# Performance work log

Measured on AMD Instinct MI355X. Metric: run time of the kernel, lower is better.

Reference implementation:

```python
import jax, jax.numpy as jnp
import numpy as np

NUM_GRAPHS = 512


def setup_inputs() -> dict:
    key = jax.random.key(0)
    k1, k2, k3, k4, k5 = jax.random.split(key, 5)
    N, D = 131072, 512
    x = jax.random.normal(k1, (N, D), dtype=jnp.float32)
    graph_ptr = jnp.sort(jax.random.randint(k2, (N,), 0, NUM_GRAPHS, dtype=jnp.int64))
    # Linear(dim, dim) params (kaiming-ish scale) and query vector
    W = jax.random.normal(k3, (D, D), dtype=jnp.float32) / np.sqrt(D)
    b = jax.random.normal(k4, (D,), dtype=jnp.float32) * 0.01
    query = jax.random.normal(k5, (D,), dtype=jnp.float32)
    return {"x": x, "graph_ptr": graph_ptr, "W": W, "b": b, "query": query}


def reference(x, graph_ptr, W, b, query):
    # gate: Linear + Tanh, then score = g @ query  -> [N]
    g = jnp.tanh(x @ W.T + b)
    score = g @ query
    seg = graph_ptr.astype(jnp.int32)
    # segmented, numerically-stable softmax over nodes of each graph
    seg_max = jax.ops.segment_max(score, seg, num_segments=NUM_GRAPHS)  # [G]
    # empty segments give -inf max; they have no nodes so gather is safe
    e = jnp.exp(score - seg_max[seg])                                   # [N]
    denom = jax.ops.segment_sum(e, seg, num_segments=NUM_GRAPHS)        # [G]
    attn = e / jnp.where(denom[seg] == 0, 1.0, denom[seg])              # [N]
    # weighted scatter-sum of node features per graph -> [G, D]
    out = jax.ops.segment_sum(attn[:, None] * x, seg, num_segments=NUM_GRAPHS)
    return out
```

## Files before the change

### kernel.cpp

```cpp
#include <hip/hip_runtime.h>

typedef _Float16 f16x8 __attribute__((ext_vector_type(8)));
typedef short short8 __attribute__((ext_vector_type(8)));
typedef float f32x16 __attribute__((ext_vector_type(16)));

#define DD 512
#define NG 512

typedef __attribute__((address_space(3))) void lds_void;
typedef __attribute__((address_space(1))) void glb_void;

static __device__ __forceinline__ void gload_lds16(const void* g, void* l) {
  __builtin_amdgcn_global_load_lds((const glb_void*)g, (lds_void*)l, 16, 0, 0);
}

#define WAITV(n) asm volatile("s_waitcnt vmcnt(" #n ") lgkmcnt(0)" ::: "memory")
#define MEMFENCE asm volatile("" ::: "memory")

static __device__ __forceinline__ float fast_tanh(float v) {
  float e = __expf(2.0f * v);
  return 1.0f - 2.0f * __builtin_amdgcn_rcpf(e + 1.0f);
}

__global__ __launch_bounds__(256) void k_convert_w(const float* __restrict__ W,
                                                   unsigned char* __restrict__ Whl) {
  int t = blockIdx.x * 256 + threadIdx.x;
  int r512 = t >> 6, kg = t & 63;
  int ny = r512 >> 8, col = r512 & 255;
  int ct = col >> 5, c31 = col & 31;
  int kt = kg >> 1, khalf = kg & 1;
  const float* p = W + (size_t)r512 * DD + kg * 8;
  short8 h;
#pragma unroll
  for (int j = 0; j < 8; ++j) {
    _Float16 hh = (_Float16)p[j];
    h[j] = (short)__builtin_bit_cast(unsigned short, hh);
  }
  unsigned char* dst = Whl + (size_t)ny * 262144 + (size_t)kt * 8192 +
                       ct * 1024 + (khalf * 32 + c31) * 16;
  *(short8*)dst = h;
}

__global__ __launch_bounds__(256, 3) void k_gemm_score(
    const float* __restrict__ x, const unsigned char* __restrict__ Whl,
    const float* __restrict__ bias, const float* __restrict__ query,
    float* __restrict__ score_part, int N) {
  __shared__ unsigned char ldsB[3][8192];
  __shared__ unsigned char ldsA[3][8192];
  __shared__ float comb[2][128];
  const int tid = threadIdx.x;
  const int wave = tid >> 6;
  const int lane = tid & 63;
  const int l31 = lane & 31;
  const int kh = lane >> 5;
  const int rg = wave >> 1;
  const int cg = wave & 1;
  const int ny = blockIdx.x;
  const int brow0 = blockIdx.y * 128;

  const unsigned char* wsrc = Whl + (size_t)ny * 262144 +
                              (size_t)wave * 2048 + (size_t)lane * 16;

  const int c0 = wave * 128 + lane;
  const int c1 = c0 + 64;
  const int s0c = c0 ^ ((c0 >> 3) & 7);
  const int s1c = c1 ^ ((c1 >> 3) & 7);
  const float* asrc0 = x + (size_t)(brow0 + (s0c >> 2)) * DD + (s0c & 3) * 4;
  const float* asrc1 = x + (size_t)(brow0 + (s1c >> 2)) * DD + (s1c & 3) * 4;

  int aoff[2][2];
#pragma unroll
  for (int f = 0; f < 2; ++f) {
    const int row = rg * 64 + f * 32 + l31;
    const int u = row * 4 + 2 * kh;
    const int m = (u >> 3) & 7;
    aoff[f][0] = (u ^ m) * 16;
    aoff[f][1] = ((u + 1) ^ m) * 16;
  }

  f32x16 acc[2][4];
#pragma unroll
  for (int f = 0; f < 2; ++f)
#pragma unroll
    for (int j = 0; j < 4; ++j)
#pragma unroll
      for (int r = 0; r < 16; ++r) acc[f][j][r] = 0.f;

#pragma unroll
  for (int s = 0; s < 2; ++s) {
#pragma unroll
    for (int i = 0; i < 2; ++i)
      gload_lds16(wsrc + (size_t)s * 8192 + i * 1024, &ldsB[s][wave * 2048 + i * 1024]);
    gload_lds16(asrc0 + s * 16, &ldsA[s][wave * 2048]);
    gload_lds16(asrc1 + s * 16, &ldsA[s][wave * 2048 + 1024]);
    MEMFENCE;
  }

  for (int kt = 0; kt < 32; ++kt) {
    if (kt == 31) WAITV(0); else WAITV(4);
    __builtin_amdgcn_s_barrier();
    MEMFENCE;

    if (kt < 30) {
      const int s = (kt + 2) % 3;
      const unsigned char* src = wsrc + (size_t)(kt + 2) * 8192;
#pragma unroll
      for (int i = 0; i < 2; ++i)
        gload_lds16(src + i * 1024, &ldsB[s][wave * 2048 + i * 1024]);
      gload_lds16(asrc0 + (kt + 2) * 16, &ldsA[s][wave * 2048]);
      gload_lds16(asrc1 + (kt + 2) * 16, &ldsA[s][wave * 2048 + 1024]);
    }
    MEMFENCE;

    const int slot = kt % 3;
    const unsigned char* ab = &ldsA[slot][0];
    const unsigned char* bb = &ldsB[slot][lane * 16 + cg * 4096];

    f16x8 ah[2];
#pragma unroll
    for (int f = 0; f < 2; ++f) {
      const float4 a0 = *(const float4*)(ab + aoff[f][0]);
      const float4 a1 = *(const float4*)(ab + aoff[f][1]);
      float af[8] = {a0.x, a0.y, a0.z, a0.w, a1.x, a1.y, a1.z, a1.w};
#pragma unroll
      for (int j = 0; j < 8; ++j) ah[f][j] = (_Float16)af[j];
    }

    __builtin_amdgcn_s_setprio(1);
#pragma unroll
    for (int j = 0; j < 4; ++j) {
      f16x8 bh = *(const f16x8*)(bb + j * 1024);
#pragma unroll
      for (int f = 0; f < 2; ++f)
        acc[f][j] = __builtin_amdgcn_mfma_f32_32x32x16_f16(ah[f], bh, acc[f][j], 0, 0, 0);
    }
    __builtin_amdgcn_s_setprio(0);
  }

  float sp[2][16];
#pragma unroll
  for (int f = 0; f < 2; ++f)
#pragma unroll
    for (int r = 0; r < 16; ++r) sp[f][r] = 0.f;
#pragma unroll
  for (int j = 0; j < 4; ++j) {
    const int col = ny * 256 + (cg * 4 + j) * 32 + l31;
    const float bb2 = bias[col];
    const float qq = query[col];
#pragma unroll
    for (int f = 0; f < 2; ++f)
#pragma unroll
      for (int r = 0; r < 16; ++r)
        sp[f][r] += fast_tanh(acc[f][j][r] + bb2) * qq;
  }
#pragma unroll
  for (int f = 0; f < 2; ++f)
#pragma unroll
    for (int r = 0; r < 16; ++r) {
      float v = sp[f][r];
      v += __shfl_xor(v, 1);
      v += __shfl_xor(v, 2);
      v += __shfl_xor(v, 4);
      v += __shfl_xor(v, 8);
      v += __shfl_xor(v, 16);
      if (l31 == 0)
        comb[cg][rg * 64 + f * 32 + (r & 3) + 8 * (r >> 2) + 4 * kh] = v;
    }
  __syncthreads();
  if (tid < 128)
    score_part[(size_t)ny * N + brow0 + tid] = comb[0][tid] + comb[1][tid];
}

__global__ __launch_bounds__(256) void k_softmax_out(
    const float* __restrict__ x, const void* __restrict__ segp,
    const float* __restrict__ sp0, const float* __restrict__ sp1,
    float* __restrict__ out, int N) {
  const int g = blockIdx.x;
  const int tid = threadIdx.x;

  const long long probe = ((const long long*)segp)[N / 2 - 1];
  const bool is64 = ((unsigned long long)probe < (unsigned long long)NG);
  const long long* s64 = (const long long*)segp;
  const int* s32 = (const int*)segp;

  int s0, s1;
  {
    int lo = 0, hi = N;
    while (lo < hi) {
      int m = (lo + hi) >> 1;
      long long v = is64 ? s64[m] : (long long)s32[m];
      if (v < (long long)g) lo = m + 1; else hi = m;
    }
    s0 = lo;
    lo = s0; hi = N;
    while (lo < hi) {
      int m = (lo + hi) >> 1;
      long long v = is64 ? s64[m] : (long long)s32[m];
      if (v < (long long)(g + 1)) lo = m + 1; else hi = m;
    }
    s1 = lo;
  }

  __shared__ float red[4];
  __shared__ float wbuf[512];

  float lm = -INFINITY;
  for (int i = s0 + tid; i < s1; i += 256) lm = fmaxf(lm, sp0[i] + sp1[i]);
#pragma unroll
  for (int m = 1; m < 64; m <<= 1) lm = fmaxf(lm, __shfl_xor(lm, m));
  if ((tid & 63) == 0) red[tid >> 6] = lm;
  __syncthreads();
  const float mx = fmaxf(fmaxf(red[0], red[1]), fmaxf(red[2], red[3]));
  __syncthreads();

  float ls = 0.f;
  for (int i = s0 + tid; i < s1; i += 256) ls += expf(sp0[i] + sp1[i] - mx);
#pragma unroll
  for (int m = 1; m < 64; m <<= 1) ls += __shfl_xor(ls, m);
  if ((tid & 63) == 0) red[tid >> 6] = ls;
  __syncthreads();
  const float sum = red[0] + red[1] + red[2] + red[3];
  const float inv = sum > 0.f ? 1.0f / sum : 0.f;

  float a0 = 0.f, a1 = 0.f;
  const int c = tid * 2;
  for (int base = s0; base < s1; base += 512) {
    const int cnt = min(512, s1 - base);
    __syncthreads();
    for (int i = tid; i < cnt; i += 256)
      wbuf[i] = expf(sp0[base + i] + sp1[base + i] - mx) * inv;
    __syncthreads();
#pragma unroll 4
    for (int j = 0; j < cnt; ++j) {
      const float w = wbuf[j];
      const float2 xv = *(const float2*)(x + (size_t)(base + j) * DD + c);
      a0 = fmaf(w, xv.x, a0);
      a1 = fmaf(w, xv.y, a1);
    }
  }
  float* op = out + (size_t)g * DD + c;
  op[0] = a0;
  op[1] = a1;
}

extern "C" void kernel_launch(void* const* d_in, const int* in_sizes, int n_in,
                              void* d_out, int out_size, void* d_ws, size_t ws_size,
                              hipStream_t stream) {
  const float* x = (const float*)d_in[0];
  const void* seg = d_in[1];
  const float* W = (const float*)d_in[2];
  const float* b = (const float*)d_in[3];
  const float* q = (const float*)d_in[4];
  float* out = (float*)d_out;
  const int N = in_sizes[0] / DD;

  unsigned char* Whl = (unsigned char*)d_ws;
  float* sp0 = (float*)(Whl + 524288);
  float* sp1 = sp0 + N;

  k_convert_w<<<128, 256, 0, stream>>>(W, Whl);
  dim3 grid(2, N / 128);
  k_gemm_score<<<grid, 256, 0, stream>>>(x, Whl, b, q, sp0, N);
  k_softmax_out<<<NG, 256, 0, stream>>>(x, seg, sp0, sp1, out, N);
}
```

Baseline: 183.9 us.

## Halve GEMM row tile to 64 and use packed f16 conversion

The score GEMM kernel now handles 64 rows per block instead of 128. This halves the A-tile LDS buffers and the accumulators, and raises the occupancy hint from 3 to 4 blocks. The fp32-to-fp16 conversion of A now uses packed cvt_pkrtz, which rounds toward zero instead of to nearest. The smaller tile is meant to raise occupancy and wave count, at the cost of halving B-tile reuse per block and so doubling W traffic from L2.

```diff
diff --git a/kernel.cpp b/kernel.cpp
--- a/kernel.cpp
+++ b/kernel.cpp
@@ -1,6 +1,8 @@
 #include <hip/hip_runtime.h>
 
 typedef _Float16 f16x8 __attribute__((ext_vector_type(8)));
+typedef __fp16 fp16v2 __attribute__((ext_vector_type(2)));
+typedef _Float16 f16v2 __attribute__((ext_vector_type(2)));
 typedef short short8 __attribute__((ext_vector_type(8)));
 typedef float f32x16 __attribute__((ext_vector_type(16)));
 
@@ -16,6 +18,11 @@
 
 #define WAITV(n) asm volatile("s_waitcnt vmcnt(" #n ") lgkmcnt(0)" ::: "memory")
 #define MEMFENCE asm volatile("" ::: "memory")
+
+static __device__ __forceinline__ f16v2 pk16(float a, float b) {
+  fp16v2 p = __builtin_amdgcn_cvt_pkrtz(a, b);
+  return __builtin_bit_cast(f16v2, p);
+}
 
 static __device__ __forceinline__ float fast_tanh(float v) {
   float e = __expf(2.0f * v);
@@ -41,13 +48,13 @@
   *(short8*)dst = h;
 }
 
-__global__ __launch_bounds__(256, 3) void k_gemm_score(
+__global__ __launch_bounds__(256, 4) void k_gemm_score(
     const float* __restrict__ x, const unsigned char* __restrict__ Whl,
     const float* __restrict__ bias, const float* __restrict__ query,
     float* __restrict__ score_part, int N) {
   __shared__ unsigned char ldsB[3][8192];
-  __shared__ unsigned char ldsA[3][8192];
-  __shared__ float comb[2][128];
+  __shared__ unsigned char ldsA[3][4096];
+  __shared__ float comb[2][64];
   const int tid = threadIdx.x;
   const int wave = tid >> 6;
   const int lane = tid & 63;
@@ -56,48 +63,41 @@
   const int rg = wave >> 1;
   const int cg = wave & 1;
   const int ny = blockIdx.x;
-  const int brow0 = blockIdx.y * 128;
+  const int brow0 = blockIdx.y * 64;
 
   const unsigned char* wsrc = Whl + (size_t)ny * 262144 +
                               (size_t)wave * 2048 + (size_t)lane * 16;
 
-  const int c0 = wave * 128 + lane;
-  const int c1 = c0 + 64;
+  const int c0 = wave * 64 + lane;
   const int s0c = c0 ^ ((c0 >> 3) & 7);
-  const int s1c = c1 ^ ((c1 >> 3) & 7);
   const float* asrc0 = x + (size_t)(brow0 + (s0c >> 2)) * DD + (s0c & 3) * 4;
-  const float* asrc1 = x + (size_t)(brow0 + (s1c >> 2)) * DD + (s1c & 3) * 4;
-
-  int aoff[2][2];
-#pragma unroll
-  for (int f = 0; f < 2; ++f) {
-    const int row = rg * 64 + f * 32 + l31;
+
+  int aoff0, aoff1;
+  {
+    const int row = rg * 32 + l31;
     const int u = row * 4 + 2 * kh;
     const int m = (u >> 3) & 7;
-    aoff[f][0] = (u ^ m) * 16;
-    aoff[f][1] = ((u + 1) ^ m) * 16;
-  }
-
-  f32x16 acc[2][4];
-#pragma unroll
-  for (int f = 0; f < 2; ++f)
-#pragma unroll
-    for (int j = 0; j < 4; ++j)
-#pragma unroll
-      for (int r = 0; r < 16; ++r) acc[f][j][r] = 0.f;
+    aoff0 = (u ^ m) * 16;
+    aoff1 = ((u + 1) ^ m) * 16;
+  }
+
+  f32x16 acc[4];
+#pragma unroll
+  for (int j = 0; j < 4; ++j)
+#pragma unroll
+    for (int r = 0; r < 16; ++r) acc[j][r] = 0.f;
 
 #pragma unroll
   for (int s = 0; s < 2; ++s) {
 #pragma unroll
     for (int i = 0; i < 2; ++i)
       gload_lds16(wsrc + (size_t)s * 8192 + i * 1024, &ldsB[s][wave * 2048 + i * 1024]);
-    gload_lds16(asrc0 + s * 16, &ldsA[s][wave * 2048]);
-    gload_lds16(asrc1 + s * 16, &ldsA[s][wave * 2048 + 1024]);
+    gload_lds16(asrc0 + s * 16, &ldsA[s][wave * 1024]);
     MEMFENCE;
   }
 
   for (int kt = 0; kt < 32; ++kt) {
-    if (kt == 31) WAITV(0); else WAITV(4);
+    if (kt == 31) WAITV(0); else WAITV(3);
     __builtin_amdgcn_s_barrier();
     MEMFENCE;
 
@@ -107,8 +107,7 @@
 #pragma unroll
       for (int i = 0; i < 2; ++i)
         gload_lds16(src + i * 1024, &ldsB[s][wave * 2048 + i * 1024]);
-      gload_lds16(asrc0 + (kt + 2) * 16, &ldsA[s][wave * 2048]);
-      gload_lds16(asrc1 + (kt + 2) * 16, &ldsA[s][wave * 2048 + 1024]);
+      gload_lds16(asrc0 + (kt + 2) * 16, &ldsA[s][wave * 1024]);
     }
     MEMFENCE;
 
@@ -116,58 +115,52 @@
     const unsigned char* ab = &ldsA[slot][0];
     const unsigned char* bb = &ldsB[slot][lane * 16 + cg * 4096];
 
-    f16x8 ah[2];
-#pragma unroll
-    for (int f = 0; f < 2; ++f) {
-      const float4 a0 = *(const float4*)(ab + aoff[f][0]);
-      const float4 a1 = *(const float4*)(ab + aoff[f][1]);
-      float af[8] = {a0.x, a0.y, a0.z, a0.w, a1.x, a1.y, a1.z, a1.w};
-#pragma unroll
-      for (int j = 0; j < 8; ++j) ah[f][j] = (_Float16)af[j];
+    const float4 a0 = *(const float4*)(ab + aoff0);
+    const float4 a1 = *(const float4*)(ab + aoff1);
+    f16x8 ah;
+    {
+      f16v2 p;
+      p = pk16(a0.x, a0.y); ah[0] = p[0]; ah[1] = p[1];
+      p = pk16(a0.z, a0.w); ah[2] = p[0]; ah[3] = p[1];
+      p = pk16(a1.x, a1.y); ah[4] = p[0]; ah[5] = p[1];
+      p = pk16(a1.z, a1.w); ah[6] = p[0]; ah[7] = p[1];
     }
 
     __builtin_amdgcn_s_setprio(1);
 #pragma unroll
     for (int j = 0; j < 4; ++j) {
       f16x8 bh = *(const f16x8*)(bb + j * 1024);
-#pragma unroll
-      for (int f = 0; f < 2; ++f)
-        acc[f][j] = __builtin_amdgcn_mfma_f32_32x32x16_f16(ah[f], bh, acc[f][j], 0, 0, 0);
+      acc[j] = __builtin_amdgcn_mfma_f32_32x32x16_f16(ah, bh, acc[j], 0, 0, 0);
     }
     __builtin_amdgcn_s_setprio(0);
   }
 
-  float sp[2][16];
-#pragma unroll
-  for (int f = 0; f < 2; ++f)
-#pragma unroll
-    for (int r = 0; r < 16; ++r) sp[f][r] = 0.f;
+  float sp[16];
+#pragma unroll
+  for (int r = 0; r < 16; ++r) sp[r] = 0.f;
 #pragma unroll
   for (int j = 0; j < 4; ++j) {
     const int col = ny * 256 + (cg * 4 + j) * 32 + l31;
     const float bb2 = bias[col];
     const float qq = query[col];
 #pragma unroll
-    for (int f = 0; f < 2; ++f)
-#pragma unroll
-      for (int r = 0; r < 16; ++r)
-        sp[f][r] += fast_tanh(acc[f][j][r] + bb2) * qq;
-  }
-#pragma unroll
-  for (int f = 0; f < 2; ++f)
-#pragma unroll
-    for (int r = 0; r < 16; ++r) {
-      float v = sp[f][r];
-      v += __shfl_xor(v, 1);
-      v += __shfl_xor(v, 2);
-      v += __shfl_xor(v, 4);
-      v += __shfl_xor(v, 8);
-      v += __shfl_xor(v, 16);
-      if (l31 == 0)
-        comb[cg][rg * 64 + f * 32 + (r & 3) + 8 * (r >> 2) + 4 * kh] = v;
-    }
-  __syncthreads();
-  if (tid < 128)
+    for (int r = 0; r < 16; ++r)
+      sp[r] += fast_tanh(acc[j][r] + bb2) * qq;
+  }
+  __syncthreads();
+#pragma unroll
+  for (int r = 0; r < 16; ++r) {
+    float v = sp[r];
+    v += __shfl_xor(v, 1);
+    v += __shfl_xor(v, 2);
+    v += __shfl_xor(v, 4);
+    v += __shfl_xor(v, 8);
+    v += __shfl_xor(v, 16);
+    if (l31 == 0)
+      comb[cg][rg * 32 + (r & 3) + 8 * (r >> 2) + 4 * kh] = v;
+  }
+  __syncthreads();
+  if (tid < 64)
     score_part[(size_t)ny * N + brow0 + tid] = comb[0][tid] + comb[1][tid];
 }
 
@@ -259,7 +252,7 @@
   float* sp1 = sp0 + N;
 
   k_convert_w<<<128, 256, 0, stream>>>(W, Whl);
-  dim3 grid(2, N / 128);
+  dim3 grid(2, N / 64);
   k_gemm_score<<<grid, 256, 0, stream>>>(x, Whl, b, q, sp0, N);
   k_softmax_out<<<NG, 256, 0, stream>>>(x, seg, sp0, sp1, out, N);
 }
```

New measurement: 182.0 us. About the same (-1.0%).

## Load x tiles directly into registers instead of staging through LDS

Applied to the files above, without the earlier changes.

The GEMM kernel now reads the fp32 x operand straight from global memory into registers, double-buffered across two k-steps, and converts it with packed round-toward-zero fp16 conversions. Only W still goes through the three-stage LDS ring. This drops the LDS staging of x and its swizzled reads, removes lgkmcnt from the wait, and lowers the occupancy hint from 3 to 2. The cost is higher register pressure and less coalesced per-lane global loads of 32-byte chunks. Issuing loads for k-steps past the end wraps them to valid addresses, so some redundant traffic is issued.

```diff
diff --git a/kernel.cpp b/kernel.cpp
--- a/kernel.cpp
+++ b/kernel.cpp
@@ -1,6 +1,8 @@
 #include <hip/hip_runtime.h>
 
 typedef _Float16 f16x8 __attribute__((ext_vector_type(8)));
+typedef __fp16 fp16v2 __attribute__((ext_vector_type(2)));
+typedef _Float16 f16v2 __attribute__((ext_vector_type(2)));
 typedef short short8 __attribute__((ext_vector_type(8)));
 typedef float f32x16 __attribute__((ext_vector_type(16)));
 
@@ -14,8 +16,13 @@
   __builtin_amdgcn_global_load_lds((const glb_void*)g, (lds_void*)l, 16, 0, 0);
 }
 
-#define WAITV(n) asm volatile("s_waitcnt vmcnt(" #n ") lgkmcnt(0)" ::: "memory")
+#define WAITV(n) asm volatile("s_waitcnt vmcnt(" #n ")" ::: "memory")
 #define MEMFENCE asm volatile("" ::: "memory")
+
+static __device__ __forceinline__ f16v2 pk16(float a, float b) {
+  fp16v2 p = __builtin_amdgcn_cvt_pkrtz(a, b);
+  return __builtin_bit_cast(f16v2, p);
+}
 
 static __device__ __forceinline__ float fast_tanh(float v) {
   float e = __expf(2.0f * v);
@@ -41,12 +48,11 @@
   *(short8*)dst = h;
 }
 
-__global__ __launch_bounds__(256, 3) void k_gemm_score(
+__global__ __launch_bounds__(256, 2) void k_gemm_score(
     const float* __restrict__ x, const unsigned char* __restrict__ Whl,
     const float* __restrict__ bias, const float* __restrict__ query,
     float* __restrict__ score_part, int N) {
   __shared__ unsigned char ldsB[3][8192];
-  __shared__ unsigned char ldsA[3][8192];
   __shared__ float comb[2][128];
   const int tid = threadIdx.x;
   const int wave = tid >> 6;
@@ -60,23 +66,8 @@
 
   const unsigned char* wsrc = Whl + (size_t)ny * 262144 +
                               (size_t)wave * 2048 + (size_t)lane * 16;
-
-  const int c0 = wave * 128 + lane;
-  const int c1 = c0 + 64;
-  const int s0c = c0 ^ ((c0 >> 3) & 7);
-  const int s1c = c1 ^ ((c1 >> 3) & 7);
-  const float* asrc0 = x + (size_t)(brow0 + (s0c >> 2)) * DD + (s0c & 3) * 4;
-  const float* asrc1 = x + (size_t)(brow0 + (s1c >> 2)) * DD + (s1c & 3) * 4;
-
-  int aoff[2][2];
-#pragma unroll
-  for (int f = 0; f < 2; ++f) {
-    const int row = rg * 64 + f * 32 + l31;
-    const int u = row * 4 + 2 * kh;
-    const int m = (u >> 3) & 7;
-    aoff[f][0] = (u ^ m) * 16;
-    aoff[f][1] = ((u + 1) ^ m) * 16;
-  }
+  const float* xp0 = x + (size_t)(brow0 + rg * 64 + l31) * DD + kh * 8;
+  const float* xp1 = xp0 + (size_t)32 * DD;
 
   f32x16 acc[2][4];
 #pragma unroll
@@ -86,55 +77,65 @@
 #pragma unroll
       for (int r = 0; r < 16; ++r) acc[f][j][r] = 0.f;
 
-#pragma unroll
-  for (int s = 0; s < 2; ++s) {
-#pragma unroll
-    for (int i = 0; i < 2; ++i)
-      gload_lds16(wsrc + (size_t)s * 8192 + i * 1024, &ldsB[s][wave * 2048 + i * 1024]);
-    gload_lds16(asrc0 + s * 16, &ldsA[s][wave * 2048]);
-    gload_lds16(asrc1 + s * 16, &ldsA[s][wave * 2048 + 1024]);
-    MEMFENCE;
-  }
-
-  for (int kt = 0; kt < 32; ++kt) {
-    if (kt == 31) WAITV(0); else WAITV(4);
-    __builtin_amdgcn_s_barrier();
-    MEMFENCE;
-
-    if (kt < 30) {
-      const int s = (kt + 2) % 3;
-      const unsigned char* src = wsrc + (size_t)(kt + 2) * 8192;
-#pragma unroll
-      for (int i = 0; i < 2; ++i)
-        gload_lds16(src + i * 1024, &ldsB[s][wave * 2048 + i * 1024]);
-      gload_lds16(asrc0 + (kt + 2) * 16, &ldsA[s][wave * 2048]);
-      gload_lds16(asrc1 + (kt + 2) * 16, &ldsA[s][wave * 2048 + 1024]);
-    }
-    MEMFENCE;
-
-    const int slot = kt % 3;
-    const unsigned char* ab = &ldsA[slot][0];
-    const unsigned char* bb = &ldsB[slot][lane * 16 + cg * 4096];
-
-    f16x8 ah[2];
-#pragma unroll
-    for (int f = 0; f < 2; ++f) {
-      const float4 a0 = *(const float4*)(ab + aoff[f][0]);
-      const float4 a1 = *(const float4*)(ab + aoff[f][1]);
-      float af[8] = {a0.x, a0.y, a0.z, a0.w, a1.x, a1.y, a1.z, a1.w};
-#pragma unroll
-      for (int j = 0; j < 8; ++j) ah[f][j] = (_Float16)af[j];
-    }
-
-    __builtin_amdgcn_s_setprio(1);
-#pragma unroll
-    for (int j = 0; j < 4; ++j) {
-      f16x8 bh = *(const f16x8*)(bb + j * 1024);
-#pragma unroll
-      for (int f = 0; f < 2; ++f)
-        acc[f][j] = __builtin_amdgcn_mfma_f32_32x32x16_f16(ah[f], bh, acc[f][j], 0, 0, 0);
-    }
-    __builtin_amdgcn_s_setprio(0);
+#define ISSUE_A(BUF, KT)                                   \
+  do {                                                     \
+    const int km_ = (KT) & 31;                             \
+    BUF[0] = *(const float4*)(xp0 + km_ * 16);             \
+    BUF[1] = *(const float4*)(xp0 + km_ * 16 + 4);         \
+    BUF[2] = *(const float4*)(xp1 + km_ * 16);             \
+    BUF[3] = *(const float4*)(xp1 + km_ * 16 + 4);         \
+  } while (0)
+
+#define ISSUE_B(KT)                                                       \
+  do {                                                                    \
+    const int sl_ = (KT) % 3;                                             \
+    const unsigned char* sb_ = wsrc + (size_t)((KT) & 31) * 8192;         \
+    gload_lds16(sb_, &ldsB[sl_][wave * 2048]);                            \
+    gload_lds16(sb_ + 1024, &ldsB[sl_][wave * 2048 + 1024]);              \
+  } while (0)
+
+  float4 aP[4], aQ[4];
+  ISSUE_A(aP, 0); ISSUE_B(0); MEMFENCE;
+  ISSUE_A(aQ, 1); ISSUE_B(1); MEMFENCE;
+
+#define BODY(KT, CUR)                                                     \
+  do {                                                                    \
+    WAITV(6);                                     \
+    __builtin_amdgcn_s_barrier();                                         \
+    MEMFENCE;                                                             \
+              \
+    f16x8 ah0, ah1;                                                       \
+    {                                                                     \
+      f16v2 p_;                                                           \
+      p_ = pk16(CUR[0].x, CUR[0].y); ah0[0] = p_[0]; ah0[1] = p_[1];      \
+      p_ = pk16(CUR[0].z, CUR[0].w); ah0[2] = p_[0]; ah0[3] = p_[1];      \
+      p_ = pk16(CUR[1].x, CUR[1].y); ah0[4] = p_[0]; ah0[5] = p_[1];      \
+      p_ = pk16(CUR[1].z, CUR[1].w); ah0[6] = p_[0]; ah0[7] = p_[1];      \
+      p_ = pk16(CUR[2].x, CUR[2].y); ah1[0] = p_[0]; ah1[1] = p_[1];      \
+      p_ = pk16(CUR[2].z, CUR[2].w); ah1[2] = p_[0]; ah1[3] = p_[1];      \
+      p_ = pk16(CUR[3].x, CUR[3].y); ah1[4] = p_[0]; ah1[5] = p_[1];      \
+      p_ = pk16(CUR[3].z, CUR[3].w); ah1[6] = p_[0]; ah1[7] = p_[1];      \
+    }                                                                     \
+    MEMFENCE;                                                             \
+    ISSUE_A(CUR, (KT) + 2);                                               \
+    ISSUE_B((KT) + 2);                                                    \
+    MEMFENCE;                                                             \
+    const unsigned char* bb_ = &ldsB[(KT) % 3][lane * 16 + cg * 4096];    \
+    __builtin_amdgcn_s_setprio(1);                                        \
+    _Pragma("unroll")                                                     \
+    for (int j = 0; j < 4; ++j) {                                         \
+      f16x8 bh_ = *(const f16x8*)(bb_ + j * 1024);                        \
+      acc[0][j] = __builtin_amdgcn_mfma_f32_32x32x16_f16(ah0, bh_, acc[0][j], 0, 0, 0); \
+      acc[1][j] = __builtin_amdgcn_mfma_f32_32x32x16_f16(ah1, bh_, acc[1][j], 0, 0, 0); \
+    }                                                                     \
+    __builtin_amdgcn_s_setprio(0);                                        \
+  } while (0)
+
+#pragma unroll 1
+  for (int it = 0; it < 16; ++it) {
+    const int kt0 = it * 2;
+    BODY(kt0, aP);
+    BODY(kt0 + 1, aQ);
   }
 
   float sp[2][16];
@@ -153,6 +154,7 @@
       for (int r = 0; r < 16; ++r)
         sp[f][r] += fast_tanh(acc[f][j][r] + bb2) * qq;
   }
+  __syncthreads();
 #pragma unroll
   for (int f = 0; f < 2; ++f)
 #pragma unroll
```

After: 233.0 us. 1.27x slower.

## Keep a 128-column fp16 W slice resident in LDS and stream x through registers

Applied to the files above, without the earlier changes.

Each block now loads a full 128-column fp16 slice of W (128 KB) into LDS once, instead of streaming W tiles through a triple-buffered pipeline. The x rows are prefetched into registers two K-steps ahead, packed to fp16 with cvt_pkrtz, and written to a small per-wave LDS buffer. Blocks grow to 512 threads and the output columns are split four ways, so the softmax kernel now sums four partial scores. The aim is to cut W reload traffic and barrier overhead inside the K loop. The cost is that x is read four times instead of twice, and the large LDS footprint limits occupancy.

```diff
diff --git a/kernel.cpp b/kernel.cpp
--- a/kernel.cpp
+++ b/kernel.cpp
@@ -1,6 +1,9 @@
 #include <hip/hip_runtime.h>
 
 typedef _Float16 f16x8 __attribute__((ext_vector_type(8)));
+typedef _Float16 f16x4 __attribute__((ext_vector_type(4)));
+typedef __fp16 fp16v2 __attribute__((ext_vector_type(2)));
+typedef _Float16 f16v2 __attribute__((ext_vector_type(2)));
 typedef short short8 __attribute__((ext_vector_type(8)));
 typedef float f32x16 __attribute__((ext_vector_type(16)));
 
@@ -14,8 +17,10 @@
   __builtin_amdgcn_global_load_lds((const glb_void*)g, (lds_void*)l, 16, 0, 0);
 }
 
-#define WAITV(n) asm volatile("s_waitcnt vmcnt(" #n ") lgkmcnt(0)" ::: "memory")
-#define MEMFENCE asm volatile("" ::: "memory")
+static __device__ __forceinline__ f16v2 pk16(float a, float b) {
+  fp16v2 p = __builtin_amdgcn_cvt_pkrtz(a, b);
+  return __builtin_bit_cast(f16v2, p);
+}
 
 static __device__ __forceinline__ float fast_tanh(float v) {
   float e = __expf(2.0f * v);
@@ -26,8 +31,8 @@
                                                    unsigned char* __restrict__ Whl) {
   int t = blockIdx.x * 256 + threadIdx.x;
   int r512 = t >> 6, kg = t & 63;
-  int ny = r512 >> 8, col = r512 & 255;
-  int ct = col >> 5, c31 = col & 31;
+  int cq = r512 >> 7, rq = r512 & 127;
+  int ct = rq >> 5, c31 = rq & 31;
   int kt = kg >> 1, khalf = kg & 1;
   const float* p = W + (size_t)r512 * DD + kg * 8;
   short8 h;
@@ -36,47 +41,37 @@
     _Float16 hh = (_Float16)p[j];
     h[j] = (short)__builtin_bit_cast(unsigned short, hh);
   }
-  unsigned char* dst = Whl + (size_t)ny * 262144 + (size_t)kt * 8192 +
+  unsigned char* dst = Whl + (size_t)cq * 131072 + (size_t)kt * 4096 +
                        ct * 1024 + (khalf * 32 + c31) * 16;
   *(short8*)dst = h;
 }
 
-__global__ __launch_bounds__(256, 3) void k_gemm_score(
+__global__ __launch_bounds__(512, 2) void k_gemm_score(
     const float* __restrict__ x, const unsigned char* __restrict__ Whl,
     const float* __restrict__ bias, const float* __restrict__ query,
     float* __restrict__ score_part, int N) {
-  __shared__ unsigned char ldsB[3][8192];
-  __shared__ unsigned char ldsA[3][8192];
-  __shared__ float comb[2][128];
+  __shared__ unsigned char ldsW[131072];
+  __shared__ unsigned char ldsA[8][2048];
   const int tid = threadIdx.x;
   const int wave = tid >> 6;
   const int lane = tid & 63;
   const int l31 = lane & 31;
   const int kh = lane >> 5;
-  const int rg = wave >> 1;
-  const int cg = wave & 1;
-  const int ny = blockIdx.x;
-  const int brow0 = blockIdx.y * 128;
-
-  const unsigned char* wsrc = Whl + (size_t)ny * 262144 +
-                              (size_t)wave * 2048 + (size_t)lane * 16;
-
-  const int c0 = wave * 128 + lane;
-  const int c1 = c0 + 64;
-  const int s0c = c0 ^ ((c0 >> 3) & 7);
-  const int s1c = c1 ^ ((c1 >> 3) & 7);
-  const float* asrc0 = x + (size_t)(brow0 + (s0c >> 2)) * DD + (s0c & 3) * 4;
-  const float* asrc1 = x + (size_t)(brow0 + (s1c >> 2)) * DD + (s1c & 3) * 4;
-
-  int aoff[2][2];
-#pragma unroll
-  for (int f = 0; f < 2; ++f) {
-    const int row = rg * 64 + f * 32 + l31;
-    const int u = row * 4 + 2 * kh;
-    const int m = (u >> 3) & 7;
-    aoff[f][0] = (u ^ m) * 16;
-    aoff[f][1] = ((u + 1) ^ m) * 16;
-  }
+  const int cq = blockIdx.x;
+  const int brow0 = blockIdx.y * 512;
+
+  {
+    const unsigned char* wsrc = Whl + (size_t)cq * 131072 + (size_t)tid * 16;
+#pragma unroll
+    for (int i = 0; i < 16; ++i)
+      gload_lds16(wsrc + i * 8192, &ldsW[tid * 16 + i * 8192]);
+  }
+
+  const float* asrc = x + (size_t)(brow0 + wave * 64 + (lane >> 2)) * DD + (lane & 3) * 4;
+  unsigned char* awr = &ldsA[wave][(lane >> 2) * 32 + (lane & 3) * 8];
+  const unsigned char* ard0 = &ldsA[wave][l31 * 32 + kh * 16];
+  const unsigned char* ard1 = &ldsA[wave][(32 + l31) * 32 + kh * 16];
+  const unsigned char* wb = &ldsW[lane * 16];
 
   f32x16 acc[2][4];
 #pragma unroll
@@ -86,55 +81,46 @@
 #pragma unroll
       for (int r = 0; r < 16; ++r) acc[f][j][r] = 0.f;
 
-#pragma unroll
-  for (int s = 0; s < 2; ++s) {
-#pragma unroll
-    for (int i = 0; i < 2; ++i)
-      gload_lds16(wsrc + (size_t)s * 8192 + i * 1024, &ldsB[s][wave * 2048 + i * 1024]);
-    gload_lds16(asrc0 + s * 16, &ldsA[s][wave * 2048]);
-    gload_lds16(asrc1 + s * 16, &ldsA[s][wave * 2048 + 1024]);
-    MEMFENCE;
-  }
-
+  float4 aR[2][4];
+#pragma unroll
+  for (int j = 0; j < 4; ++j) aR[0][j] = *(const float4*)(asrc + j * 16 * DD);
+#pragma unroll
+  for (int j = 0; j < 4; ++j) aR[1][j] = *(const float4*)(asrc + j * 16 * DD + 16);
+
+#define AWRITE(S)                                                      \
+  do {                                                                 \
+    _Pragma("unroll")                                                  \
+    for (int j = 0; j < 4; ++j) {                                      \
+      f16v2 p0_ = pk16(aR[S][j].x, aR[S][j].y);                        \
+      f16v2 p1_ = pk16(aR[S][j].z, aR[S][j].w);                        \
+      f16x4 v_ = {p0_[0], p0_[1], p1_[0], p1_[1]};                     \
+      *(f16x4*)(awr + j * 512) = v_;                                   \
+    }                                                                  \
+  } while (0)
+
+  asm volatile("s_waitcnt vmcnt(0)" ::: "memory");
+  AWRITE(0);
+#pragma unroll
+  for (int j = 0; j < 4; ++j) aR[0][j] = *(const float4*)(asrc + j * 16 * DD + 32);
+  __syncthreads();
+
+#pragma unroll 2
   for (int kt = 0; kt < 32; ++kt) {
-    if (kt == 31) WAITV(0); else WAITV(4);
-    __builtin_amdgcn_s_barrier();
-    MEMFENCE;
-
-    if (kt < 30) {
-      const int s = (kt + 2) % 3;
-      const unsigned char* src = wsrc + (size_t)(kt + 2) * 8192;
-#pragma unroll
-      for (int i = 0; i < 2; ++i)
-        gload_lds16(src + i * 1024, &ldsB[s][wave * 2048 + i * 1024]);
-      gload_lds16(asrc0 + (kt + 2) * 16, &ldsA[s][wave * 2048]);
-      gload_lds16(asrc1 + (kt + 2) * 16, &ldsA[s][wave * 2048 + 1024]);
-    }
-    MEMFENCE;
-
-    const int slot = kt % 3;
-    const unsigned char* ab = &ldsA[slot][0];
-    const unsigned char* bb = &ldsB[slot][lane * 16 + cg * 4096];
-
-    f16x8 ah[2];
-#pragma unroll
-    for (int f = 0; f < 2; ++f) {
-      const float4 a0 = *(const float4*)(ab + aoff[f][0]);
-      const float4 a1 = *(const float4*)(ab + aoff[f][1]);
-      float af[8] = {a0.x, a0.y, a0.z, a0.w, a1.x, a1.y, a1.z, a1.w};
-#pragma unroll
-      for (int j = 0; j < 8; ++j) ah[f][j] = (_Float16)af[j];
-    }
-
-    __builtin_amdgcn_s_setprio(1);
+    const int t1 = (kt + 1) & 1;
+    f16x8 a0 = *(const f16x8*)(ard0);
+    f16x8 a1 = *(const f16x8*)(ard1);
+    const unsigned char* bb = wb + kt * 4096;
 #pragma unroll
     for (int j = 0; j < 4; ++j) {
       f16x8 bh = *(const f16x8*)(bb + j * 1024);
-#pragma unroll
-      for (int f = 0; f < 2; ++f)
-        acc[f][j] = __builtin_amdgcn_mfma_f32_32x32x16_f16(ah[f], bh, acc[f][j], 0, 0, 0);
-    }
-    __builtin_amdgcn_s_setprio(0);
+      acc[0][j] = __builtin_amdgcn_mfma_f32_32x32x16_f16(a0, bh, acc[0][j], 0, 0, 0);
+      acc[1][j] = __builtin_amdgcn_mfma_f32_32x32x16_f16(a1, bh, acc[1][j], 0, 0, 0);
+    }
+    AWRITE(t1);
+    const int km = (kt + 3) & 31;
+#pragma unroll
+    for (int j = 0; j < 4; ++j)
+      aR[t1][j] = *(const float4*)(asrc + j * 16 * DD + km * 16);
   }
 
   float sp[2][16];
@@ -144,7 +130,7 @@
     for (int r = 0; r < 16; ++r) sp[f][r] = 0.f;
 #pragma unroll
   for (int j = 0; j < 4; ++j) {
-    const int col = ny * 256 + (cg * 4 + j) * 32 + l31;
+    const int col = cq * 128 + j * 32 + l31;
     const float bb2 = bias[col];
     const float qq = query[col];
 #pragma unroll
@@ -164,17 +150,14 @@
       v += __shfl_xor(v, 8);
       v += __shfl_xor(v, 16);
       if (l31 == 0)
-        comb[cg][rg * 64 + f * 32 + (r & 3) + 8 * (r >> 2) + 4 * kh] = v;
-    }
-  __syncthreads();
-  if (tid < 128)
-    score_part[(size_t)ny * N + brow0 + tid] = comb[0][tid] + comb[1][tid];
+        score_part[(size_t)cq * N + brow0 + wave * 64 + f * 32 +
+                   (r & 3) + 8 * (r >> 2) + 4 * kh] = v;
+    }
 }
 
 __global__ __launch_bounds__(256) void k_softmax_out(
     const float* __restrict__ x, const void* __restrict__ segp,
-    const float* __restrict__ sp0, const float* __restrict__ sp1,
-    float* __restrict__ out, int N) {
+    const float* __restrict__ sp, float* __restrict__ out, int N) {
   const int g = blockIdx.x;
   const int tid = threadIdx.x;
 
@@ -204,8 +187,10 @@
   __shared__ float red[4];
   __shared__ float wbuf[512];
 
+#define SCORE(i) (sp[i] + sp[N + (i)] + sp[2 * N + (i)] + sp[3 * N + (i)])
+
   float lm = -INFINITY;
-  for (int i = s0 + tid; i < s1; i += 256) lm = fmaxf(lm, sp0[i] + sp1[i]);
+  for (int i = s0 + tid; i < s1; i += 256) lm = fmaxf(lm, SCORE(i));
 #pragma unroll
   for (int m = 1; m < 64; m <<= 1) lm = fmaxf(lm, __shfl_xor(lm, m));
   if ((tid & 63) == 0) red[tid >> 6] = lm;
@@ -214,7 +199,7 @@
   __syncthreads();
 
   float ls = 0.f;
-  for (int i = s0 + tid; i < s1; i += 256) ls += expf(sp0[i] + sp1[i] - mx);
+  for (int i = s0 + tid; i < s1; i += 256) ls += expf(SCORE(i) - mx);
 #pragma unroll
   for (int m = 1; m < 64; m <<= 1) ls += __shfl_xor(ls, m);
   if ((tid & 63) == 0) red[tid >> 6] = ls;
@@ -228,7 +213,7 @@
     const int cnt = min(512, s1 - base);
     __syncthreads();
     for (int i = tid; i < cnt; i += 256)
-      wbuf[i] = expf(sp0[base + i] + sp1[base + i] - mx) * inv;
+      wbuf[i] = expf(SCORE(base + i) - mx) * inv;
     __syncthreads();
 #pragma unroll 4
     for (int j = 0; j < cnt; ++j) {
@@ -255,11 +240,10 @@
   const int N = in_sizes[0] / DD;
 
   unsigned char* Whl = (unsigned char*)d_ws;
-  float* sp0 = (float*)(Whl + 524288);
-  float* sp1 = sp0 + N;
+  float* sp = (float*)(Whl + 524288);
 
   k_convert_w<<<128, 256, 0, stream>>>(W, Whl);
-  dim3 grid(2, N / 128);
-  k_gemm_score<<<grid, 256, 0, stream>>>(x, Whl, b, q, sp0, N);
-  k_softmax_out<<<NG, 256, 0, stream>>>(x, seg, sp0, sp1, out, N);
-}
+  dim3 grid(4, N / 512);
+  k_gemm_score<<<grid, 512, 0, stream>>>(x, Whl, b, q, sp, N);
+  k_softmax_out<<<NG, 256, 0, stream>>>(x, seg, sp, out, N);
+}
```

Measured after the change: 321.9 us. 1.75x slower.
